# Performance work log

Hardware: AMD Instinct MI355X
Metric: run time of the kernel (lower is better)

The kernel has to match this reference:

```python
import jax, jax.numpy as jnp
import numpy as np

N_NODES = 20000
N_EDGES = 160000
D = 1000          # out_channels of GatedGraphConv / Linear in-dim
NUM_LAYERS = 3


def setup_inputs() -> dict:
    key = jax.random.key(0)
    ks = jax.random.split(key, 10)
    x = jax.random.normal(ks[0], (N_NODES, D), dtype=jnp.float32)
    edge_index = jax.random.randint(ks[1], (2, N_EDGES), 0, N_NODES, dtype=jnp.int32)
    edge_weight = jax.random.uniform(ks[2], (N_EDGES,), dtype=jnp.float32)
    s = 1.0 / np.sqrt(D)
    weight = jax.random.uniform(ks[3], (NUM_LAYERS, D, D), minval=-s, maxval=s, dtype=jnp.float32)
    w_ih = jax.random.uniform(ks[4], (3 * D, D), minval=-s, maxval=s, dtype=jnp.float32)
    w_hh = jax.random.uniform(ks[5], (3 * D, D), minval=-s, maxval=s, dtype=jnp.float32)
    b_ih = jax.random.uniform(ks[6], (3 * D,), minval=-s, maxval=s, dtype=jnp.float32)
    b_hh = jax.random.uniform(ks[7], (3 * D,), minval=-s, maxval=s, dtype=jnp.float32)
    fc_w = jax.random.uniform(ks[8], (1, D), minval=-s, maxval=s, dtype=jnp.float32)
    fc_b = jax.random.uniform(ks[9], (1,), minval=-s, maxval=s, dtype=jnp.float32)
    return {
        "x": x, "edge_index": edge_index, "edge_weight": edge_weight,
        "weight": weight, "w_ih": w_ih, "w_hh": w_hh, "b_ih": b_ih, "b_hh": b_hh,
        "fc_w": fc_w, "fc_b": fc_b, "prob": 0,
    }


def _gru_cell(m, h, w_ih, w_hh, b_ih, b_hh):
    # torch.nn.GRUCell: gate order r, z, n
    gi = m @ w_ih.T + b_ih   # [N, 3D]
    gh = h @ w_hh.T + b_hh   # [N, 3D]
    i_r, i_z, i_n = jnp.split(gi, 3, axis=-1)
    h_r, h_z, h_n = jnp.split(gh, 3, axis=-1)
    r = jax.nn.sigmoid(i_r + h_r)
    z = jax.nn.sigmoid(i_z + h_z)
    n = jnp.tanh(i_n + r * h_n)
    return (1.0 - z) * n + z * h


def reference(x, edge_index, edge_weight, weight, w_ih, w_hh, b_ih, b_hh, fc_w, fc_b, prob):
    src = edge_index[0]
    dst = edge_index[1]
    h = x
    for layer in range(NUM_LAYERS):
        m = h @ weight[layer]                                  # [N, D]
        msg = m[src] * edge_weight[:, None]                    # [E, D]
        agg = jax.ops.segment_sum(msg, dst, num_segments=N_NODES)  # scatter-add
        h = _gru_cell(agg, h, w_ih, w_hh, b_ih, b_hh)
    h = jax.nn.relu(h)
    # F.dropout with p=prob=0 is identity (scale 1/(1-0)=1)
    return h @ fc_w.T + fc_b                                   # [N, 1]
```

## Files before the change

kernel.cpp:

```cpp
#include <hip/hip_runtime.h>

typedef unsigned short u16;
typedef unsigned int u32;
typedef __attribute__((ext_vector_type(8))) short bf16x8;
typedef __attribute__((ext_vector_type(4))) float f32x4;

#define N_NODES 20000
#define N_EDGES 160000
#define DDIM    1000
#define KP      1024
#define SP      41200000
#define WCAT_L  6291456

__device__ __forceinline__ float b2f(u16 u) {
    union { u32 i; float f; } v; v.i = ((u32)u) << 16; return v.f;
}
__device__ __forceinline__ u16 f2b(float f) {
    union { float f; u32 i; } v; v.f = f;
    u32 r = v.i + 0x7FFFu + ((v.i >> 16) & 1u);
    return (u16)(r >> 16);
}
__device__ __forceinline__ u32 pack2(float a, float b) {
    return (u32)f2b(a) | ((u32)f2b(b) << 16);
}
__device__ __forceinline__ f32x4 mfma16(bf16x8 a, bf16x8 b, f32x4 c) {
    return __builtin_amdgcn_mfma_f32_16x16x32_bf16(a, b, c, 0, 0, 0);
}
__device__ __forceinline__ float fexp_(float x) {
    return __builtin_amdgcn_exp2f(x * 1.4426950408889634f);
}
__device__ __forceinline__ float fsigmoid_(float x) {
    return __builtin_amdgcn_rcpf(1.0f + fexp_(-x));
}
__device__ __forceinline__ float ftanh_(float x) {
    float ax = fabsf(x);
    float e = fexp_(-2.0f * ax);
    float t = (1.0f - e) * __builtin_amdgcn_rcpf(1.0f + e);
    return x >= 0.0f ? t : -t;
}

__device__ __forceinline__ void gl2lds16(const u16* g, u16* l) {
    __builtin_amdgcn_global_load_lds(
        (const __attribute__((address_space(1))) u32*)g,
        (__attribute__((address_space(3))) u32*)l, 16, 0, 0);
}

__global__ __launch_bounds__(256) void cvt_rows(const float* __restrict__ in,
                                                u16* __restrict__ out) {
    int r = blockIdx.x, c = threadIdx.x * 4;
    u32 o[2] = {0, 0};
    if (c < DDIM) {
        float4 v = *(const float4*)(in + (size_t)r * DDIM + c);
        o[0] = pack2(v.x, v.y); o[1] = pack2(v.z, v.w);
    }
    *(uint2*)(out + (size_t)r * KP + c) = *(const uint2*)o;
}

__global__ __launch_bounds__(256) void cvt_weights(const float* __restrict__ wih,
                                                   const float* __restrict__ W,
                                                   const float* __restrict__ whh,
                                                   u16* __restrict__ wihb,
                                                   u16* __restrict__ Wb3,
                                                   u16* __restrict__ wcat) {
    int b = blockIdx.x, c = threadIdx.x * 4;
    const float* src;
    u16* dst;
    if (b < 3000) {
        src = wih + (size_t)b * DDIM;
        dst = wihb + (size_t)b * KP;
    } else if (b < 6000) {
        int r = b - 3000;
        int l = r / 1000, row = r - l * 1000;
        src = W + (size_t)r * DDIM;
        dst = Wb3 + (size_t)l * 1048576 + (size_t)row * KP;
    } else {
        int r = b - 6000;
        int l = r / 3000, gr = r - l * 3000;
        int g = gr / 1000, n2 = gr - g * 1000;
        src = whh + (size_t)gr * DDIM;
        dst = wcat + (size_t)l * WCAT_L + ((size_t)g * 1024 + n2) * 2048 + 1024;
    }
    u32 o[2] = {0, 0};
    if (c < DDIM) {
        float4 v = *(const float4*)(src + c);
        o[0] = pack2(v.x, v.y); o[1] = pack2(v.z, v.w);
    }
    *(uint2*)(dst + c) = *(const uint2*)o;
}

__global__ __launch_bounds__(256) void count_edges(const int* __restrict__ ei,
                                                   int* __restrict__ cnt) {
    int e = blockIdx.x * 256 + threadIdx.x;
    if (e < N_EDGES) atomicAdd(&cnt[ei[N_EDGES + e]], 1);
}

__global__ __launch_bounds__(1024) void scan_offsets(const int* __restrict__ cnt,
                                                     int* __restrict__ ofs) {
    __shared__ int s[1024];
    const int CH = 20;
    int t = threadIdx.x;
    int base = t * CH;
    int loc[CH];
    int sum = 0;
    for (int j = 0; j < CH; j++) {
        int i = base + j;
        loc[j] = sum;
        sum += (i < N_NODES) ? cnt[i] : 0;
    }
    s[t] = sum;
    __syncthreads();
    for (int d = 1; d < 1024; d <<= 1) {
        int v = (t >= d) ? s[t - d] : 0;
        __syncthreads();
        s[t] += v;
        __syncthreads();
    }
    int excl = s[t] - sum;
    for (int j = 0; j < CH; j++) {
        int i = base + j;
        if (i < N_NODES) ofs[i] = excl + loc[j];
    }
    if (t == 0) ofs[N_NODES] = N_EDGES;
}

__global__ __launch_bounds__(256) void fill_buckets(const int* __restrict__ ei,
                                                    const int* __restrict__ ofs,
                                                    int* __restrict__ cur,
                                                    int* __restrict__ bkt) {
    int e = blockIdx.x * 256 + threadIdx.x;
    if (e >= N_EDGES) return;
    int d = ei[N_EDGES + e];
    int pos = atomicAdd(&cur[d], 1);
    bkt[ofs[d] + pos] = e;
}

__global__ __launch_bounds__(256) void node_agg(const int* __restrict__ ei,
                                                const float* __restrict__ ew,
                                                const int* __restrict__ ofs,
                                                const int* __restrict__ bkt,
                                                const u16* __restrict__ hsrc,
                                                u16* __restrict__ agg) {
    __shared__ int   s_src[2][32];
    __shared__ float s_w[2][32];
    __shared__ int   s_it[2];
    int tid = threadIdx.x;
    int half = tid >> 7, t = tid & 127;
    int node = blockIdx.x * 2 + half;
    int beg = ofs[node], end = ofs[node + 1];
    if (t == 0) s_it[half] = (end - beg + 31) >> 5;
    __syncthreads();
    int iters = max(s_it[0], s_it[1]);
    float acc[8] = {};
    for (int it = 0; it < iters; it++) {
        int cb = beg + it * 32;
        int n = min(32, end - cb);
        if (t < n) {
            int e = bkt[cb + t];
            s_src[half][t] = ei[e];
            s_w[half][t]   = ew[e];
        }
        __syncthreads();
        if (t < 125) {
            for (int j = 0; j < n; j++) {
                int src = s_src[half][j];
                float w = s_w[half][j];
                uint4 v = *(const uint4*)(hsrc + (size_t)src * KP + t * 8);
                const u16* p = (const u16*)&v;
#pragma unroll
                for (int k = 0; k < 8; k++) acc[k] += b2f(p[k]) * w;
            }
        }
        __syncthreads();
    }
    if (t < 125) {
        u32 o[4] = {pack2(acc[0], acc[1]), pack2(acc[2], acc[3]),
                    pack2(acc[4], acc[5]), pack2(acc[6], acc[7])};
        *(uint4*)(agg + (size_t)node * KP + t * 8) = *(const uint4*)o;
    } else if (t < 128) {
        uint4 z = {0, 0, 0, 0};
        *(uint4*)(agg + (size_t)node * KP + 1000 + (t - 125) * 8) = z;
    }
}

__global__ __launch_bounds__(256) void gemm_wc(const u16* __restrict__ A,
                                               const u16* __restrict__ Bt3,
                                               u16* __restrict__ wcat) {
    __shared__ u16 S[16384];
    int tid = threadIdx.x;
    int lane = tid & 63, wave = tid >> 6;
    int wr = wave >> 1, wc = wave & 1;
    int bid = blockIdx.x;
    int l = blockIdx.y;
    int m0 = (bid >> 3) * 128, n0 = (bid & 7) * 128;
    const u16* Bt = Bt3 + (size_t)l * 1048576;

    int aoff[4], boff[4];
#pragma unroll
    for (int i = 0; i < 4; i++) {
        int c = tid + 256 * i;
        int row = c >> 3, sl = c & 7;
        int kc = sl ^ (row & 7);
        aoff[i] = (m0 + row) * KP + kc * 8;
        boff[i] = (n0 + row) * KP + kc * 8;
    }
    f32x4 acc[4][4] = {};
    int fr = lane & 15, q = lane >> 4, sw = fr & 7;

    for (int k0 = 0; k0 < KP; k0 += 64) {
#pragma unroll
        for (int i = 0; i < 4; i++) {
            gl2lds16(A + aoff[i] + k0, &S[tid * 8 + 2048 * i]);
            gl2lds16(Bt + boff[i] + k0, &S[8192 + tid * 8 + 2048 * i]);
        }
        __syncthreads();
#pragma unroll
        for (int ks = 0; ks < 2; ks++) {
            int kx = ((ks * 4 + q) ^ sw) * 8;
            bf16x8 af[4], bf[4];
#pragma unroll
            for (int i = 0; i < 4; i++)
                af[i] = *(const bf16x8*)&S[(wr * 64 + i * 16 + fr) * 64 + kx];
#pragma unroll
            for (int j = 0; j < 4; j++)
                bf[j] = *(const bf16x8*)&S[8192 + (wc * 64 + j * 16 + fr) * 64 + kx];
#pragma unroll
            for (int i = 0; i < 4; i++)
#pragma unroll
                for (int j = 0; j < 4; j++)
                    acc[i][j] = mfma16(af[i], bf[j], acc[i][j]);
        }
        __syncthreads();
    }

    u16* wl = wcat + (size_t)l * WCAT_L;
    int cc = lane & 15, r4 = q * 4;
#pragma unroll
    for (int i = 0; i < 4; i++)
#pragma unroll
        for (int j = 0; j < 4; j++) {
            int gn = n0 + wc * 64 + j * 16 + cc;
            if (gn >= DDIM) continue;
#pragma unroll
            for (int r = 0; r < 4; r++) {
                int gm = m0 + wr * 64 + i * 16 + r4 + r;
                if (gm >= 3000) continue;
                int slab = (gm >= 2000) ? 2 : (gm >= 1000 ? 1 : 0);
                int row = gm - slab * 1000;
                wl[(size_t)slab * 2097152 + (size_t)row * 2048 + gn] =
                    f2b(acc[i][j][r]);
            }
        }
}

__global__ __launch_bounds__(512, 2) void gru_fused(const u16* __restrict__ agg,
                                                    const u16* __restrict__ h,
                                                    const u16* __restrict__ wcat,
                                                    const float* __restrict__ bih,
                                                    const float* __restrict__ bhh,
                                                    u16* __restrict__ hout) {
    extern __shared__ u16 S[];
    int tid = threadIdx.x;
    int lane = tid & 63, wave = tid >> 6;

    int bid = blockIdx.x;
    int xcd = bid & 7;
    int s = bid >> 3;
    int panel = s >> 1, hi = s & 1;
    int m0 = panel * 256;
    int n0 = (xcd * 2 + hi) * 64;

    int aoff[4];
#pragma unroll
    for (int i = 0; i < 4; i++) {
        int c = tid + 512 * i;
        int row = c >> 3, sl = c & 7;
        int kc = sl ^ (row & 7);
        aoff[i] = (m0 + row) * KP + kc * 8;
    }
    int wrow = tid >> 3;
    int woff = (n0 + wrow) * 2048 + ((tid & 7) ^ (wrow & 7)) * 8;

    f32x4 aR[2][4] = {}, aZ[2][4] = {}, aN[2][4] = {}, aH[2][4] = {};
    int fr = lane & 15, q = lane >> 4, sw = fr & 7;
    int arow = (wave * 32 + fr) * 64;
    int wfr = fr * 64;
    int kx0 = (q ^ sw) * 8, kx1 = ((4 + q) ^ sw) * 8;

#define STAGE_W(ts, wb) do {                                                  \
        int kw_ = (ts) * 64;                                                  \
        _Pragma("unroll")                                                     \
        for (int g_ = 0; g_ < 3; g_++)                                        \
            gl2lds16(wcat + (size_t)g_ * 2097152 + woff + kw_,                \
                     &S[49152 + (wb) * 12288 + g_ * 4096 + tid * 8]);         \
    } while (0)

#define STAGE_A2(ts, ab, r0) do {                                             \
        const u16* ap_ = ((ts) < 16) ? agg : h;                               \
        int kb_ = ((ts) < 16) ? (ts) * 64 : (ts) * 64 - 1024;                 \
        _Pragma("unroll")                                                     \
        for (int i_ = (r0); i_ < (r0) + 2; i_++)                              \
            gl2lds16(ap_ + aoff[i_] + kb_,                                    \
                     &S[(ab) * 16384 + tid * 8 + 4096 * i_]);                 \
    } while (0)

#define READ_WF(g_) do {                                                      \
        _Pragma("unroll")                                                     \
        for (int j_ = 0; j_ < 4; j_++) {                                      \
            wf[j_][0] = *(const bf16x8*)&S[Wb + (g_) * 4096 + wfr + j_ * 1024 + kx0]; \
            wf[j_][1] = *(const bf16x8*)&S[Wb + (g_) * 4096 + wfr + j_ * 1024 + kx1]; \
        }                                                                     \
    } while (0)

#define MFMA_PH(ACC) do {                                                     \
        __builtin_amdgcn_s_setprio(1);                                        \
        _Pragma("unroll")                                                     \
        for (int i_ = 0; i_ < 2; i_++)                                        \
            _Pragma("unroll")                                                 \
            for (int j_ = 0; j_ < 4; j_++) {                                  \
                ACC[i_][j_] = mfma16(af[i_][0], wf[j_][0], ACC[i_][j_]);      \
                ACC[i_][j_] = mfma16(af[i_][1], wf[j_][1], ACC[i_][j_]);      \
            }                                                                 \
        __builtin_amdgcn_s_setprio(0);                                        \
    } while (0)

    STAGE_A2(0, 0, 0); STAGE_A2(0, 0, 2);
    STAGE_W(0, 0);
    STAGE_A2(1, 1, 0); STAGE_A2(1, 1, 2);
    asm volatile("s_waitcnt vmcnt(4)" ::: "memory");
    __builtin_amdgcn_s_barrier();

    int abuf = 0;
#pragma unroll 1
    for (int t = 0; t < 32; t++) {
        int Ab = abuf * 16384;
        int Wb = 49152 + (t & 1) * 12288;
        bf16x8 af[2][2], wf[4][2];
#pragma unroll
        for (int i_ = 0; i_ < 2; i_++) {
            af[i_][0] = *(const bf16x8*)&S[Ab + arow + i_ * 1024 + kx0];
            af[i_][1] = *(const bf16x8*)&S[Ab + arow + i_ * 1024 + kx1];
        }
        READ_WF(0);
        if (t <= 30) STAGE_W(t + 1, (t + 1) & 1);
        __builtin_amdgcn_s_barrier();
        MFMA_PH(aR);
        __builtin_amdgcn_s_barrier();
        READ_WF(1);
        int anext = abuf + 2; if (anext >= 3) anext -= 3;
        if (t <= 29) STAGE_A2(t + 2, anext, 0);
        __builtin_amdgcn_s_barrier();
        MFMA_PH(aZ);
        __builtin_amdgcn_s_barrier();
        READ_WF(2);
        if (t <= 29) STAGE_A2(t + 2, anext, 2);
        __builtin_amdgcn_s_barrier();
        if (t < 16) MFMA_PH(aN); else MFMA_PH(aH);
        if (t <= 29)      asm volatile("s_waitcnt vmcnt(4)" ::: "memory");
        else if (t == 30) asm volatile("s_waitcnt vmcnt(0)" ::: "memory");
        __builtin_amdgcn_s_barrier();
        abuf++; if (abuf == 3) abuf = 0;
    }
#undef STAGE_W
#undef STAGE_A2
#undef READ_WF
#undef MFMA_PH

    int cc = lane & 15, r4 = q * 4;
#pragma unroll
    for (int j = 0; j < 4; j++) {
        int gn = n0 + j * 16 + cc;
        if (gn >= DDIM) continue;
        float br  = bih[gn] + bhh[gn];
        float bz  = bih[1000 + gn] + bhh[1000 + gn];
        float bni = bih[2000 + gn];
        float bnh = bhh[2000 + gn];
#pragma unroll
        for (int i = 0; i < 2; i++)
#pragma unroll
            for (int r = 0; r < 4; r++) {
                int gm = m0 + wave * 32 + i * 16 + r4 + r;
                if (gm >= N_NODES) continue;
                float rg = fsigmoid_(aR[i][j][r] + br);
                float zg = fsigmoid_(aZ[i][j][r] + bz);
                float ng = ftanh_(aN[i][j][r] + bni + rg * (aH[i][j][r] + bnh));
                size_t idx = (size_t)gm * KP + gn;
                float hp = b2f(h[idx]);
                hout[idx] = f2b((1.0f - zg) * ng + zg * hp);
            }
    }
}

__global__ __launch_bounds__(256) void fc_out(const u16* __restrict__ h,
                                              const float* __restrict__ fw,
                                              const float* __restrict__ fb,
                                              float* __restrict__ out) {
    int row = blockIdx.x * 4 + (threadIdx.x >> 6);
    int lane = threadIdx.x & 63;
    if (row >= N_NODES) return;
    float s = 0.0f;
#pragma unroll
    for (int i = 0; i < 2; i++) {
        int c = lane + 64 * i;
        if (c < 125) {
            uint4 v = *(const uint4*)(h + (size_t)row * KP + c * 8);
            const u16* pv = (const u16*)&v;
            float4 w0 = *(const float4*)(fw + c * 8);
            float4 w1 = *(const float4*)(fw + c * 8 + 4);
            const float* wp = (const float*)&w0;
            float hv;
#pragma unroll
            for (int k = 0; k < 4; k++) {
                hv = b2f(pv[k]);
                s += (hv > 0.0f ? hv : 0.0f) * wp[k];
            }
            wp = (const float*)&w1;
#pragma unroll
            for (int k = 0; k < 4; k++) {
                hv = b2f(pv[4 + k]);
                s += (hv > 0.0f ? hv : 0.0f) * wp[k];
            }
        }
    }
    for (int off = 32; off > 0; off >>= 1) s += __shfl_down(s, off, 64);
    if (lane == 0) out[row] = s + fb[0];
}

extern "C" void kernel_launch(void* const* d_in, const int* in_sizes, int n_in,
                              void* d_out, int out_size, void* d_ws, size_t ws_size,
                              hipStream_t stream) {
    const float* x   = (const float*)d_in[0];
    const int*   ei  = (const int*)d_in[1];
    const float* ew  = (const float*)d_in[2];
    const float* W   = (const float*)d_in[3];
    const float* wih = (const float*)d_in[4];
    const float* whh = (const float*)d_in[5];
    const float* bih = (const float*)d_in[6];
    const float* bhh = (const float*)d_in[7];
    const float* fw  = (const float*)d_in[8];
    const float* fb  = (const float*)d_in[9];
    float* out = (float*)d_out;

    hipFuncSetAttribute((const void*)gru_fused,
                        hipFuncAttributeMaxDynamicSharedMemorySize, 147456);

    char* ws = (char*)d_ws;
    u16* xb   = (u16*)(ws);
    u16* bufA = (u16*)(ws + (size_t)SP);
    u16* bufB = (u16*)(ws + (size_t)2 * SP);
    u16* wcat = (u16*)(ws + 123600000);
    int* cnt  = (int*)(ws + 161400000);
    int* cur  = (int*)(ws + 161480000);
    int* ofs  = (int*)(ws + 161560000);
    int* bkt  = (int*)(ws + 161640192);

    u16* wihb = bufA;
    u16* Wb3  = bufA + 3145728;

    cvt_rows<<<N_NODES, 256, 0, stream>>>(x, xb);
    cvt_weights<<<15000, 256, 0, stream>>>(wih, W, whh, wihb, Wb3, wcat);
    gemm_wc<<<dim3(192, 3), 256, 0, stream>>>(wihb, Wb3, wcat);
    hipMemsetAsync(cnt, 0, 160000, stream);
    count_edges<<<625, 256, 0, stream>>>(ei, cnt);
    scan_offsets<<<1, 1024, 0, stream>>>(cnt, ofs);
    fill_buckets<<<625, 256, 0, stream>>>(ei, ofs, cur, bkt);

    node_agg<<<10000, 256, 0, stream>>>(ei, ew, ofs, bkt, xb, bufB);
    gru_fused<<<1264, 512, 147456, stream>>>(bufB, xb, wcat, bih, bhh, bufA);

    node_agg<<<10000, 256, 0, stream>>>(ei, ew, ofs, bkt, bufA, bufB);
    gru_fused<<<1264, 512, 147456, stream>>>(bufB, bufA, wcat + WCAT_L, bih, bhh, xb);

    node_agg<<<10000, 256, 0, stream>>>(ei, ew, ofs, bkt, xb, bufB);
    gru_fused<<<1264, 512, 147456, stream>>>(bufB, xb, wcat + 2 * WCAT_L, bih, bhh, bufA);

    fc_out<<<5000, 256, 0, stream>>>(bufA, fw, fb, out);
}
```

Before: 1.219 ms.

## Retile GRU waves to a 4x2 grid and drop intra-iteration barriers

```diff
diff --git a/kernel.cpp b/kernel.cpp
--- a/kernel.cpp
+++ b/kernel.cpp
@@ -261,6 +261,7 @@
     extern __shared__ u16 S[];
     int tid = threadIdx.x;
     int lane = tid & 63, wave = tid >> 6;
+    int wr = wave >> 1, wc = wave & 1;
 
     int bid = blockIdx.x;
     int xcd = bid & 7;
@@ -280,11 +281,14 @@
     int wrow = tid >> 3;
     int woff = (n0 + wrow) * 2048 + ((tid & 7) ^ (wrow & 7)) * 8;
 
-    f32x4 aR[2][4] = {}, aZ[2][4] = {}, aN[2][4] = {}, aH[2][4] = {};
+    f32x4 aR[4][2] = {}, aZ[4][2] = {}, aN[4][2] = {}, aH[4][2] = {};
     int fr = lane & 15, q = lane >> 4, sw = fr & 7;
-    int arow = (wave * 32 + fr) * 64;
-    int wfr = fr * 64;
     int kx0 = (q ^ sw) * 8, kx1 = ((4 + q) ^ sw) * 8;
+    int arow[4], wcol[2];
+#pragma unroll
+    for (int i = 0; i < 4; i++) arow[i] = (wr * 64 + i * 16 + fr) * 64;
+#pragma unroll
+    for (int j = 0; j < 2; j++) wcol[j] = (wc * 32 + j * 16 + fr) * 64;
 
 #define STAGE_W(ts, wb) do {                                                  \
         int kw_ = (ts) * 64;                                                  \
@@ -305,22 +309,20 @@
 
 #define READ_WF(g_) do {                                                      \
         _Pragma("unroll")                                                     \
-        for (int j_ = 0; j_ < 4; j_++) {                                      \
-            wf[j_][0] = *(const bf16x8*)&S[Wb + (g_) * 4096 + wfr + j_ * 1024 + kx0]; \
-            wf[j_][1] = *(const bf16x8*)&S[Wb + (g_) * 4096 + wfr + j_ * 1024 + kx1]; \
+        for (int j_ = 0; j_ < 2; j_++) {                                      \
+            wf[j_][0] = *(const bf16x8*)&S[Wb + (g_) * 4096 + wcol[j_] + kx0];\
+            wf[j_][1] = *(const bf16x8*)&S[Wb + (g_) * 4096 + wcol[j_] + kx1];\
         }                                                                     \
     } while (0)
 
-#define MFMA_PH(ACC) do {                                                     \
-        __builtin_amdgcn_s_setprio(1);                                        \
+#define MFMA_G(ACC) do {                                                      \
         _Pragma("unroll")                                                     \
-        for (int i_ = 0; i_ < 2; i_++)                                        \
+        for (int i_ = 0; i_ < 4; i_++)                                        \
             _Pragma("unroll")                                                 \
-            for (int j_ = 0; j_ < 4; j_++) {                                  \
+            for (int j_ = 0; j_ < 2; j_++) {                                  \
                 ACC[i_][j_] = mfma16(af[i_][0], wf[j_][0], ACC[i_][j_]);      \
                 ACC[i_][j_] = mfma16(af[i_][1], wf[j_][1], ACC[i_][j_]);      \
             }                                                                 \
-        __builtin_amdgcn_s_setprio(0);                                        \
     } while (0)
 
     STAGE_A2(0, 0, 0); STAGE_A2(0, 0, 2);
@@ -334,27 +336,22 @@
     for (int t = 0; t < 32; t++) {
         int Ab = abuf * 16384;
         int Wb = 49152 + (t & 1) * 12288;
-        bf16x8 af[2][2], wf[4][2];
-#pragma unroll
-        for (int i_ = 0; i_ < 2; i_++) {
-            af[i_][0] = *(const bf16x8*)&S[Ab + arow + i_ * 1024 + kx0];
-            af[i_][1] = *(const bf16x8*)&S[Ab + arow + i_ * 1024 + kx1];
+        int anext = abuf + 2; if (anext >= 3) anext -= 3;
+        bf16x8 af[4][2], wf[2][2];
+#pragma unroll
+        for (int i = 0; i < 4; i++) {
+            af[i][0] = *(const bf16x8*)&S[Ab + arow[i] + kx0];
+            af[i][1] = *(const bf16x8*)&S[Ab + arow[i] + kx1];
         }
         READ_WF(0);
         if (t <= 30) STAGE_W(t + 1, (t + 1) & 1);
-        __builtin_amdgcn_s_barrier();
-        MFMA_PH(aR);
-        __builtin_amdgcn_s_barrier();
+        MFMA_G(aR);
         READ_WF(1);
-        int anext = abuf + 2; if (anext >= 3) anext -= 3;
         if (t <= 29) STAGE_A2(t + 2, anext, 0);
-        __builtin_amdgcn_s_barrier();
-        MFMA_PH(aZ);
-        __builtin_amdgcn_s_barrier();
+        MFMA_G(aZ);
         READ_WF(2);
         if (t <= 29) STAGE_A2(t + 2, anext, 2);
-        __builtin_amdgcn_s_barrier();
-        if (t < 16) MFMA_PH(aN); else MFMA_PH(aH);
+        if (t < 16) MFMA_G(aN); else MFMA_G(aH);
         if (t <= 29)      asm volatile("s_waitcnt vmcnt(4)" ::: "memory");
         else if (t == 30) asm volatile("s_waitcnt vmcnt(0)" ::: "memory");
         __builtin_amdgcn_s_barrier();
@@ -363,22 +360,22 @@
 #undef STAGE_W
 #undef STAGE_A2
 #undef READ_WF
-#undef MFMA_PH
+#undef MFMA_G
 
     int cc = lane & 15, r4 = q * 4;
 #pragma unroll
-    for (int j = 0; j < 4; j++) {
-        int gn = n0 + j * 16 + cc;
+    for (int j = 0; j < 2; j++) {
+        int gn = n0 + wc * 32 + j * 16 + cc;
         if (gn >= DDIM) continue;
         float br  = bih[gn] + bhh[gn];
         float bz  = bih[1000 + gn] + bhh[1000 + gn];
         float bni = bih[2000 + gn];
         float bnh = bhh[2000 + gn];
 #pragma unroll
-        for (int i = 0; i < 2; i++)
+        for (int i = 0; i < 4; i++)
 #pragma unroll
             for (int r = 0; r < 4; r++) {
-                int gm = m0 + wave * 32 + i * 16 + r4 + r;
+                int gm = m0 + wr * 64 + i * 16 + r4 + r;
                 if (gm >= N_NODES) continue;
                 float rg = fsigmoid_(aR[i][j][r] + br);
                 float zg = fsigmoid_(aZ[i][j][r] + bz);
```

After: 1.104 ms, median of 2. 9.4% less time.
